# Kernel tuning notes

Hardware: AMD Instinct MI355X
Metric: run time of the kernel (lower is better)

Reference implementation:

```python
import jax, jax.numpy as jnp
import numpy as np
import math


def setup_inputs() -> dict:
    key = jax.random.key(0)
    k1, k2 = jax.random.split(key)
    q = jax.random.normal(k1, (2, 8, 2048, 64), dtype=jnp.float32)
    v = jax.random.normal(k2, (2, 8, 2048, 64), dtype=jnp.float32)
    return {"q": q, "v": v}


def reference(q, v):
    # q, v: [B, H, L, D]. Softmax-free Gaussian-kernel attention.
    # squared L2 distance via expanded form: ||qi||^2 + ||qj||^2 - 2 qi.qj
    # (same math as the original's broadcasted difference, without the
    #  O(B,H,L,L,D) intermediate)
    d = q.shape[-1]
    sq = jnp.sum(q * q, axis=-1)                      # [B, H, L]
    dots = jnp.einsum('bhid,bhjd->bhij', q, q)        # [B, H, L, L]
    sq_l2 = sq[..., :, None] + sq[..., None, :] - 2.0 * dots
    score = jnp.exp(-1.0 / (2.0 * math.sqrt(d)) * sq_l2)  # [B, H, L, L]
    return jnp.einsum('bhij,bhjd->bhid', score, v)    # [B, H, L, D]
```

## Files before the change

kernel.cpp:

```cpp
#include <hip/hip_runtime.h>
#include <hip/hip_bf16.h>
#include <stdint.h>

typedef __bf16 bf16_t;
typedef bf16_t bf16x8 __attribute__((ext_vector_type(8)));
typedef float f32x16 __attribute__((ext_vector_type(16)));
typedef float fvec4 __attribute__((ext_vector_type(4)));
typedef unsigned int u32x4v __attribute__((ext_vector_type(4)));

#define LEN 2048
#define DIM 64
#define QBLK 128
#define KVB 64

#define C_L8  0.18033688011112043f
#define C_L16 0.09016844005556021f

__device__ __forceinline__ float fexp2(float x) {
#if __has_builtin(__builtin_amdgcn_exp2f)
  return __builtin_amdgcn_exp2f(x);
#else
  return exp2f(x);
#endif
}

__device__ __forceinline__ unsigned pk2(float lo, float hi) {
  union { bf16_t h; unsigned short u; } a, b;
  a.h = (bf16_t)lo; b.h = (bf16_t)hi;
  return (unsigned)a.u | ((unsigned)b.u << 16);
}

__device__ __forceinline__ int sw(int row, int byte) {
  return row * 128 + (byte ^ ((row & 7) << 4));
}

__global__ __launch_bounds__(512, 2) void soft_attn(
    const float* __restrict__ q, const float* __restrict__ v,
    float* __restrict__ out) {
  __shared__ __align__(16) char smem[33280];

  const int tid    = threadIdx.x;
  const int lane   = tid & 63;
  const int wave   = tid >> 6;
  const int rg     = wave & 3;
  const int parity = wave >> 2;
  const int tp     = tid & 255;
  const int g      = lane >> 5;
  const int nn     = lane & 31;

  const int wg = ((blockIdx.x & 7) << 5) | (blockIdx.x >> 3);
  const int bh = wg >> 4;
  const int qb = wg & 15;

  const float* qh = q + (size_t)bh * LEN * DIM;
  const float* vh = v + (size_t)bh * LEN * DIM;

  char*  kbufp = smem + parity * 8192;
  char*  vbufp = smem + 16384 + parity * 8192;
  float* wkp   = (float*)(smem + 32768) + parity * 64;

  const int qrow = qb * QBLK + rg * 32 + nn;
  bf16x8 qf[4];
  float sq = 0.f;
  {
    const float* qp = qh + (size_t)qrow * DIM;
#pragma unroll
    for (int kc = 0; kc < 4; ++kc) {
      const int d0 = kc * 16 + g * 8;
      fvec4 x = *(const fvec4*)(qp + d0);
      fvec4 y = *(const fvec4*)(qp + d0 + 4);
      bf16x8 t;
#pragma unroll
      for (int e = 0; e < 4; ++e) {
        bf16_t h0 = (bf16_t)x[e]; t[e]     = h0; float f0 = (float)h0; sq += f0 * f0;
        bf16_t h1 = (bf16_t)y[e]; t[e + 4] = h1; float f1 = (float)h1; sq += f1 * f1;
      }
      qf[kc] = t;
    }
  }
  sq += __shfl_xor(sq, 32);
  const float hq = sq * C_L16;

  f32x16 acc0 = {};
  f32x16 acc1 = {};

  for (int it = 0; it < 16; ++it) {
    const int jt = it * 2 + parity;
    const float* kg = qh + (size_t)jt * KVB * DIM;
    const float* vg = vh + (size_t)jt * KVB * DIM;

    __syncthreads();

#pragma unroll
    for (int s = 0; s < 2; ++s) {
      const int c  = tp + 256 * s;
      const int j  = c >> 3;
      const int d0 = (c & 7) * 8;
      fvec4 x = *(const fvec4*)(kg + j * DIM + d0);
      fvec4 y = *(const fvec4*)(kg + j * DIM + d0 + 4);
      bf16x8 t; float p = 0.f;
#pragma unroll
      for (int e = 0; e < 4; ++e) {
        bf16_t h0 = (bf16_t)x[e]; t[e]     = h0; float f0 = (float)h0; p += f0 * f0;
        bf16_t h1 = (bf16_t)y[e]; t[e + 4] = h1; float f1 = (float)h1; p += f1 * f1;
      }
      *(bf16x8*)(kbufp + sw(j, d0 * 2)) = t;
      p += __shfl_xor(p, 1);
      p += __shfl_xor(p, 2);
      p += __shfl_xor(p, 4);
      if ((lane & 7) == 0) wkp[j] = fexp2(-p * C_L16);
    }

    __syncthreads();

    float vl[2][8];
    const int vd = tp & 63;
    const int vw = tp >> 6;
#pragma unroll
    for (int s = 0; s < 2; ++s) {
      const int j0 = vw * 8 + 32 * s;
      const float* vp = vg + j0 * DIM + vd;
#pragma unroll
      for (int r = 0; r < 8; ++r) vl[s][r] = vp[r * DIM];
    }

    bf16x8 af[4];
#pragma unroll
    for (int jsub = 0; jsub < 2; ++jsub) {
      f32x16 t = {};
#pragma unroll
      for (int kc = 0; kc < 4; ++kc) {
        bf16x8 kf = *(const bf16x8*)(kbufp + sw(jsub * 32 + nn, kc * 32 + g * 16));
        t = __builtin_amdgcn_mfma_f32_32x32x16_bf16(kf, qf[kc], t, 0, 0, 0);
      }
      unsigned P[8];
#pragma unroll
      for (int e = 0; e < 8; ++e) {
        float s0 = fexp2(__builtin_fmaf(t[2 * e],     C_L8, -hq));
        float s1 = fexp2(__builtin_fmaf(t[2 * e + 1], C_L8, -hq));
        P[e] = pk2(s0, s1);
      }
      asm volatile("v_permlane32_swap_b32 %0, %1" : "+v"(P[0]), "+v"(P[2]));
      asm volatile("v_permlane32_swap_b32 %0, %1" : "+v"(P[1]), "+v"(P[3]));
      asm volatile("v_permlane32_swap_b32 %0, %1" : "+v"(P[4]), "+v"(P[6]));
      asm volatile("v_permlane32_swap_b32 %0, %1" : "+v"(P[5]), "+v"(P[7]));
      u32x4v f0v = { P[0], P[1], P[2], P[3] };
      u32x4v f1v = { P[4], P[5], P[6], P[7] };
      af[jsub * 2]     = __builtin_bit_cast(bf16x8, f0v);
      af[jsub * 2 + 1] = __builtin_bit_cast(bf16x8, f1v);
    }

#pragma unroll
    for (int s = 0; s < 2; ++s) {
      const int j0 = vw * 8 + 32 * s;
      bf16x8 t;
#pragma unroll
      for (int r = 0; r < 8; ++r) {
        float w = wkp[j0 + r];
        t[r] = (bf16_t)(vl[s][r] * w);
      }
      *(bf16x8*)(vbufp + sw(vd, j0 * 2)) = t;
    }

    __syncthreads();

#pragma unroll
    for (int kc = 0; kc < 4; ++kc) {
      bf16x8 v0 = *(const bf16x8*)(vbufp + sw(nn,      kc * 32 + g * 16));
      bf16x8 v1 = *(const bf16x8*)(vbufp + sw(32 + nn, kc * 32 + g * 16));
      acc0 = __builtin_amdgcn_mfma_f32_32x32x16_bf16(af[kc], v0, acc0, 0, 0, 0);
      acc1 = __builtin_amdgcn_mfma_f32_32x32x16_bf16(af[kc], v1, acc1, 0, 0, 0);
    }
  }

  __syncthreads();
  float* xb = (float*)smem + rg * 2048;
  if (parity == 1) {
#pragma unroll
    for (int r = 0; r < 16; ++r) {
      xb[r * 64 + lane]        = acc0[r];
      xb[(16 + r) * 64 + lane] = acc1[r];
    }
  }
  __syncthreads();
  if (parity == 0) {
    float* op = out + ((size_t)bh * LEN + qb * QBLK + rg * 32) * DIM;
#pragma unroll
    for (int r = 0; r < 16; ++r) {
      const int row = (r & 3) + 8 * (r >> 2) + 4 * g;
      op[(size_t)row * DIM + nn]      = acc0[r] + xb[r * 64 + lane];
      op[(size_t)row * DIM + 32 + nn] = acc1[r] + xb[(16 + r) * 64 + lane];
    }
  }
}

extern "C" void kernel_launch(void* const* d_in, const int* in_sizes, int n_in,
                              void* d_out, int out_size, void* d_ws, size_t ws_size,
                              hipStream_t stream) {
  const float* q = (const float*)d_in[0];
  const float* v = (const float*)d_in[1];
  float* out = (float*)d_out;
  (void)in_sizes; (void)n_in; (void)d_ws; (void)ws_size; (void)out_size;
  soft_attn<<<dim3(256), dim3(512), 0, stream>>>(q, v, out);
}
```

Before: 106.5 us.

## Add bf16 prepass kernel and double-buffered async-LDS main attention kernel

Adds a prepass that converts Q/K to bf16 once, computes the squared norms, and stores V pre-scaled by exp(-||k||^2) and transposed into the workspace. The main kernel then streams bf16 K and V^T tiles directly into LDS through global_load_lds, double-buffered so the next tile loads while the current one computes. It splits the KV loop across four waves per query group and uses 64-row query blocks with 512 workgroups. The aim is to drop the per-block redundant fp32 conversion and the extra barriers. In exchange it pays for a second launch and a round trip through workspace memory, and it falls back to the old kernel when the workspace is too small.

```diff
diff --git a/kernel.cpp b/kernel.cpp
--- a/kernel.cpp
+++ b/kernel.cpp
@@ -10,8 +10,7 @@
 
 #define LEN 2048
 #define DIM 64
-#define QBLK 128
-#define KVB 64
+#define NH  16
 
 #define C_L8  0.18033688011112043f
 #define C_L16 0.09016844005556021f
@@ -30,36 +29,229 @@
   return (unsigned)a.u | ((unsigned)b.u << 16);
 }
 
-__device__ __forceinline__ int sw(int row, int byte) {
+__device__ __forceinline__ void glds16(const void* g, void* l) {
+  __builtin_amdgcn_global_load_lds(
+      (const __attribute__((address_space(1))) void*)g,
+      (__attribute__((address_space(3))) void*)l, 16, 0, 0);
+}
+
+__device__ __forceinline__ int swk(int row, int b) {
+  return row * 128 + (b ^ ((row & 7) << 4));
+}
+__device__ __forceinline__ int swv(int row, int b) {
+  return row * 256 + (b ^ ((row & 7) << 4));
+}
+
+__global__ __launch_bounds__(256) void prepass(
+    const float* __restrict__ q, const float* __restrict__ v,
+    bf16_t* __restrict__ kb, bf16_t* __restrict__ vt, float* __restrict__ sqw) {
+  __shared__ float wlds[64];
+  const int b = blockIdx.x;
+  const int h = b >> 5, jb = b & 31;
+  const int t = threadIdx.x;
+  const float* qh = q + ((size_t)h * LEN + jb * 64) * DIM;
+  const float* vh = v + ((size_t)h * LEN + jb * 64) * DIM;
+
+  {
+    const int j = t >> 2, d0 = (t & 3) * 16;
+    const float* qp = qh + j * DIM + d0;
+    float s = 0.f;
+    bf16x8 o0, o1;
+#pragma unroll
+    for (int e = 0; e < 8; ++e) {
+      bf16_t hh = (bf16_t)qp[e]; o0[e] = hh; float f = (float)hh; s += f * f;
+    }
+#pragma unroll
+    for (int e = 0; e < 8; ++e) {
+      bf16_t hh = (bf16_t)qp[8 + e]; o1[e] = hh; float f = (float)hh; s += f * f;
+    }
+    bf16_t* kp = kb + ((size_t)h * LEN + jb * 64 + j) * DIM + d0;
+    *(bf16x8*)kp = o0;
+    *(bf16x8*)(kp + 8) = o1;
+    s += __shfl_xor(s, 1);
+    s += __shfl_xor(s, 2);
+    if ((t & 3) == 0) {
+      wlds[j] = fexp2(-s * C_L16);
+      sqw[h * LEN + jb * 64 + j] = s * C_L16;
+    }
+  }
+  __syncthreads();
+  {
+    const int d = t & 63, jg = t >> 6;
+    float vv[16];
+#pragma unroll
+    for (int e = 0; e < 16; ++e) vv[e] = vh[(jg * 16 + e) * DIM + d];
+    bf16x8 o0, o1;
+#pragma unroll
+    for (int e = 0; e < 8; ++e)  o0[e] = (bf16_t)(vv[e] * wlds[jg * 16 + e]);
+#pragma unroll
+    for (int e = 0; e < 8; ++e)  o1[e] = (bf16_t)(vv[8 + e] * wlds[jg * 16 + 8 + e]);
+    bf16_t* vp = vt + ((size_t)h * DIM + d) * LEN + jb * 64 + jg * 16;
+    *(bf16x8*)vp = o0;
+    *(bf16x8*)(vp + 8) = o1;
+  }
+}
+
+__global__ __launch_bounds__(512, 4) void soft_attn_main(
+    const bf16_t* __restrict__ kb, const bf16_t* __restrict__ vt,
+    const float* __restrict__ sqw, float* __restrict__ out) {
+  __shared__ __align__(16) char smem[65536];
+
+  const int tid  = threadIdx.x;
+  const int lane = tid & 63;
+  const int wave = tid >> 6;
+  const int rg   = wave & 1;
+  const int par  = wave >> 1;
+  const int g    = lane >> 5;
+  const int nn   = lane & 31;
+
+  const int b  = blockIdx.x;
+  const int wg = ((b & 7) << 6) | (b >> 3);
+  const int bh = wg >> 5;
+  const int qb = wg & 31;
+
+  const bf16_t* kh  = kb + (size_t)bh * LEN * DIM;
+  const bf16_t* vth = vt + (size_t)bh * DIM * LEN;
+
+  const int qrow = qb * 64 + rg * 32 + nn;
+  bf16x8 qf[4];
+  {
+    const bf16_t* qp = kh + (size_t)qrow * DIM;
+#pragma unroll
+    for (int kc = 0; kc < 4; ++kc)
+      qf[kc] = *(const bf16x8*)(qp + kc * 16 + g * 8);
+  }
+  const float hq = sqw[bh * LEN + qrow];
+
+  const bf16_t* ksrc[2];
+  const bf16_t* vsrc[2];
+#pragma unroll
+  for (int s = 0; s < 2; ++s) {
+    const int krow = wave * 16 + s * 8 + (lane >> 3);
+    const int kby  = ((lane & 7) * 16) ^ ((lane >> 3) << 4);
+    ksrc[s] = kh + (size_t)krow * DIM + (kby >> 1);
+    const int vrow = wave * 8 + s * 4 + (lane >> 4);
+    const int vby  = ((lane & 15) * 16) ^ ((vrow & 7) << 4);
+    vsrc[s] = vth + (size_t)vrow * LEN + (vby >> 1);
+  }
+  char* kdst = smem + wave * 2048;
+  char* vdst = smem + 32768 + wave * 2048;
+
+  f32x16 acc0 = {};
+  f32x16 acc1 = {};
+
+#pragma unroll
+  for (int s = 0; s < 2; ++s) {
+    glds16(ksrc[s], kdst + s * 1024);
+    glds16(vsrc[s], vdst + s * 1024);
+  }
+  __syncthreads();
+
+  int buf = 0;
+  for (int it = 0; it < 16; ++it) {
+    if (it + 1 < 16) {
+      const int nb = buf ^ 1;
+#pragma unroll
+      for (int s = 0; s < 2; ++s) {
+        glds16(ksrc[s] + (size_t)(it + 1) * 128 * DIM, kdst + nb * 16384 + s * 1024);
+        glds16(vsrc[s] + (size_t)(it + 1) * 128,       vdst + nb * 16384 + s * 1024);
+      }
+    }
+
+    const char* kb0 = smem + buf * 16384;
+    const char* vb0 = smem + 32768 + buf * 16384;
+
+    f32x16 t = {};
+#pragma unroll
+    for (int kc = 0; kc < 4; ++kc) {
+      bf16x8 kf = *(const bf16x8*)(kb0 + swk(par * 32 + nn, kc * 32 + g * 16));
+      t = __builtin_amdgcn_mfma_f32_32x32x16_bf16(kf, qf[kc], t, 0, 0, 0);
+    }
+
+    unsigned P[8];
+#pragma unroll
+    for (int e = 0; e < 8; ++e) {
+      float s0 = fexp2(__builtin_fmaf(t[2 * e],     C_L8, -hq));
+      float s1 = fexp2(__builtin_fmaf(t[2 * e + 1], C_L8, -hq));
+      P[e] = pk2(s0, s1);
+    }
+    asm volatile("v_permlane32_swap_b32 %0, %1" : "+v"(P[0]), "+v"(P[2]));
+    asm volatile("v_permlane32_swap_b32 %0, %1" : "+v"(P[1]), "+v"(P[3]));
+    asm volatile("v_permlane32_swap_b32 %0, %1" : "+v"(P[4]), "+v"(P[6]));
+    asm volatile("v_permlane32_swap_b32 %0, %1" : "+v"(P[5]), "+v"(P[7]));
+    u32x4v f0v = { P[0], P[1], P[2], P[3] };
+    u32x4v f1v = { P[4], P[5], P[6], P[7] };
+    bf16x8 af0 = __builtin_bit_cast(bf16x8, f0v);
+    bf16x8 af1 = __builtin_bit_cast(bf16x8, f1v);
+
+    {
+      bf16x8 v0 = *(const bf16x8*)(vb0 + swv(nn,      par * 64 + g * 16));
+      bf16x8 v1 = *(const bf16x8*)(vb0 + swv(32 + nn, par * 64 + g * 16));
+      acc0 = __builtin_amdgcn_mfma_f32_32x32x16_bf16(af0, v0, acc0, 0, 0, 0);
+      acc1 = __builtin_amdgcn_mfma_f32_32x32x16_bf16(af0, v1, acc1, 0, 0, 0);
+      v0 = *(const bf16x8*)(vb0 + swv(nn,      par * 64 + 32 + g * 16));
+      v1 = *(const bf16x8*)(vb0 + swv(32 + nn, par * 64 + 32 + g * 16));
+      acc0 = __builtin_amdgcn_mfma_f32_32x32x16_bf16(af1, v0, acc0, 0, 0, 0);
+      acc1 = __builtin_amdgcn_mfma_f32_32x32x16_bf16(af1, v1, acc1, 0, 0, 0);
+    }
+
+    __syncthreads();
+    buf ^= 1;
+  }
+
+  float* xb = (float*)smem;
+  if (par != 0) {
+    float* dst = xb + ((par - 1) * 2 + rg) * 2048;
+#pragma unroll
+    for (int r = 0; r < 16; ++r) {
+      dst[r * 64 + lane]        = acc0[r];
+      dst[(16 + r) * 64 + lane] = acc1[r];
+    }
+  }
+  __syncthreads();
+  if (par == 0) {
+    float* op = out + ((size_t)bh * LEN + qb * 64 + rg * 32) * DIM;
+#pragma unroll
+    for (int r = 0; r < 16; ++r) {
+      const int row = (r & 3) + 8 * (r >> 2) + 4 * g;
+      float a0 = acc0[r], a1 = acc1[r];
+#pragma unroll
+      for (int p = 1; p < 4; ++p) {
+        const float* sb = xb + ((p - 1) * 2 + rg) * 2048;
+        a0 += sb[r * 64 + lane];
+        a1 += sb[(16 + r) * 64 + lane];
+      }
+      op[(size_t)row * DIM + nn]      = a0;
+      op[(size_t)row * DIM + 32 + nn] = a1;
+    }
+  }
+}
+
+__device__ __forceinline__ int swfb(int row, int byte) {
   return row * 128 + (byte ^ ((row & 7) << 4));
 }
 
-__global__ __launch_bounds__(512, 2) void soft_attn(
+__global__ __launch_bounds__(512, 2) void soft_attn_fb(
     const float* __restrict__ q, const float* __restrict__ v,
     float* __restrict__ out) {
   __shared__ __align__(16) char smem[33280];
-
-  const int tid    = threadIdx.x;
-  const int lane   = tid & 63;
-  const int wave   = tid >> 6;
-  const int rg     = wave & 3;
+  const int tid = threadIdx.x;
+  const int lane = tid & 63;
+  const int wave = tid >> 6;
+  const int rg = wave & 3;
   const int parity = wave >> 2;
-  const int tp     = tid & 255;
-  const int g      = lane >> 5;
-  const int nn     = lane & 31;
-
+  const int tp = tid & 255;
+  const int g = lane >> 5;
+  const int nn = lane & 31;
   const int wg = ((blockIdx.x & 7) << 5) | (blockIdx.x >> 3);
   const int bh = wg >> 4;
   const int qb = wg & 15;
-
   const float* qh = q + (size_t)bh * LEN * DIM;
   const float* vh = v + (size_t)bh * LEN * DIM;
-
-  char*  kbufp = smem + parity * 8192;
-  char*  vbufp = smem + 16384 + parity * 8192;
-  float* wkp   = (float*)(smem + 32768) + parity * 64;
-
-  const int qrow = qb * QBLK + rg * 32 + nn;
+  char* kbufp = smem + parity * 8192;
+  char* vbufp = smem + 16384 + parity * 8192;
+  float* wkp = (float*)(smem + 32768) + parity * 64;
+  const int qrow = qb * 128 + rg * 32 + nn;
   bf16x8 qf[4];
   float sq = 0.f;
   {
@@ -72,7 +264,7 @@
       bf16x8 t;
 #pragma unroll
       for (int e = 0; e < 4; ++e) {
-        bf16_t h0 = (bf16_t)x[e]; t[e]     = h0; float f0 = (float)h0; sq += f0 * f0;
+        bf16_t h0 = (bf16_t)x[e]; t[e] = h0; float f0 = (float)h0; sq += f0 * f0;
         bf16_t h1 = (bf16_t)y[e]; t[e + 4] = h1; float f1 = (float)h1; sq += f1 * f1;
       }
       qf[kc] = t;
@@ -80,39 +272,33 @@
   }
   sq += __shfl_xor(sq, 32);
   const float hq = sq * C_L16;
-
   f32x16 acc0 = {};
   f32x16 acc1 = {};
-
   for (int it = 0; it < 16; ++it) {
     const int jt = it * 2 + parity;
-    const float* kg = qh + (size_t)jt * KVB * DIM;
-    const float* vg = vh + (size_t)jt * KVB * DIM;
-
+    const float* kg = qh + (size_t)jt * 64 * DIM;
+    const float* vg = vh + (size_t)jt * 64 * DIM;
     __syncthreads();
-
 #pragma unroll
     for (int s = 0; s < 2; ++s) {
-      const int c  = tp + 256 * s;
-      const int j  = c >> 3;
+      const int c = tp + 256 * s;
+      const int j = c >> 3;
       const int d0 = (c & 7) * 8;
       fvec4 x = *(const fvec4*)(kg + j * DIM + d0);
       fvec4 y = *(const fvec4*)(kg + j * DIM + d0 + 4);
       bf16x8 t; float p = 0.f;
 #pragma unroll
       for (int e = 0; e < 4; ++e) {
-        bf16_t h0 = (bf16_t)x[e]; t[e]     = h0; float f0 = (float)h0; p += f0 * f0;
+        bf16_t h0 = (bf16_t)x[e]; t[e] = h0; float f0 = (float)h0; p += f0 * f0;
         bf16_t h1 = (bf16_t)y[e]; t[e + 4] = h1; float f1 = (float)h1; p += f1 * f1;
       }
-      *(bf16x8*)(kbufp + sw(j, d0 * 2)) = t;
+      *(bf16x8*)(kbufp + swfb(j, d0 * 2)) = t;
       p += __shfl_xor(p, 1);
       p += __shfl_xor(p, 2);
       p += __shfl_xor(p, 4);
       if ((lane & 7) == 0) wkp[j] = fexp2(-p * C_L16);
     }
-
     __syncthreads();
-
     float vl[2][8];
     const int vd = tp & 63;
     const int vw = tp >> 6;
@@ -123,20 +309,19 @@
 #pragma unroll
       for (int r = 0; r < 8; ++r) vl[s][r] = vp[r * DIM];
     }
-
     bf16x8 af[4];
 #pragma unroll
     for (int jsub = 0; jsub < 2; ++jsub) {
       f32x16 t = {};
 #pragma unroll
       for (int kc = 0; kc < 4; ++kc) {
-        bf16x8 kf = *(const bf16x8*)(kbufp + sw(jsub * 32 + nn, kc * 32 + g * 16));
+        bf16x8 kf = *(const bf16x8*)(kbufp + swfb(jsub * 32 + nn, kc * 32 + g * 16));
         t = __builtin_amdgcn_mfma_f32_32x32x16_bf16(kf, qf[kc], t, 0, 0, 0);
       }
       unsigned P[8];
 #pragma unroll
       for (int e = 0; e < 8; ++e) {
-        float s0 = fexp2(__builtin_fmaf(t[2 * e],     C_L8, -hq));
+        float s0 = fexp2(__builtin_fmaf(t[2 * e], C_L8, -hq));
         float s1 = fexp2(__builtin_fmaf(t[2 * e + 1], C_L8, -hq));
         P[e] = pk2(s0, s1);
       }
@@ -146,10 +331,9 @@
       asm volatile("v_permlane32_swap_b32 %0, %1" : "+v"(P[5]), "+v"(P[7]));
       u32x4v f0v = { P[0], P[1], P[2], P[3] };
       u32x4v f1v = { P[4], P[5], P[6], P[7] };
-      af[jsub * 2]     = __builtin_bit_cast(bf16x8, f0v);
+      af[jsub * 2] = __builtin_bit_cast(bf16x8, f0v);
       af[jsub * 2 + 1] = __builtin_bit_cast(bf16x8, f1v);
     }
-
 #pragma unroll
     for (int s = 0; s < 2; ++s) {
       const int j0 = vw * 8 + 32 * s;
@@ -159,36 +343,33 @@
         float w = wkp[j0 + r];
         t[r] = (bf16_t)(vl[s][r] * w);
       }
-      *(bf16x8*)(vbufp + sw(vd, j0 * 2)) = t;
-    }
-
+      *(bf16x8*)(vbufp + swfb(vd, j0 * 2)) = t;
+    }
     __syncthreads();
-
 #pragma unroll
     for (int kc = 0; kc < 4; ++kc) {
-      bf16x8 v0 = *(const bf16x8*)(vbufp + sw(nn,      kc * 32 + g * 16));
-      bf16x8 v1 = *(const bf16x8*)(vbufp + sw(32 + nn, kc * 32 + g * 16));
+      bf16x8 v0 = *(const bf16x8*)(vbufp + swfb(nn, kc * 32 + g * 16));
+      bf16x8 v1 = *(const bf16x8*)(vbufp + swfb(32 + nn, kc * 32 + g * 16));
       acc0 = __builtin_amdgcn_mfma_f32_32x32x16_bf16(af[kc], v0, acc0, 0, 0, 0);
       acc1 = __builtin_amdgcn_mfma_f32_32x32x16_bf16(af[kc], v1, acc1, 0, 0, 0);
     }
   }
-
   __syncthreads();
   float* xb = (float*)smem + rg * 2048;
   if (parity == 1) {
 #pragma unroll
     for (int r = 0; r < 16; ++r) {
-      xb[r * 64 + lane]        = acc0[r];
+      xb[r * 64 + lane] = acc0[r];
       xb[(16 + r) * 64 + lane] = acc1[r];
     }
   }
   __syncthreads();
   if (parity == 0) {
-    float* op = out + ((size_t)bh * LEN + qb * QBLK + rg * 32) * DIM;
+    float* op = out + ((size_t)bh * LEN + qb * 128 + rg * 32) * DIM;
 #pragma unroll
     for (int r = 0; r < 16; ++r) {
       const int row = (r & 3) + 8 * (r >> 2) + 4 * g;
-      op[(size_t)row * DIM + nn]      = acc0[r] + xb[r * 64 + lane];
+      op[(size_t)row * DIM + nn] = acc0[r] + xb[r * 64 + lane];
       op[(size_t)row * DIM + 32 + nn] = acc1[r] + xb[(16 + r) * 64 + lane];
     }
   }
@@ -200,6 +381,17 @@
   const float* q = (const float*)d_in[0];
   const float* v = (const float*)d_in[1];
   float* out = (float*)d_out;
-  (void)in_sizes; (void)n_in; (void)d_ws; (void)ws_size; (void)out_size;
-  soft_attn<<<dim3(256), dim3(512), 0, stream>>>(q, v, out);
-}
+  (void)in_sizes; (void)n_in; (void)out_size;
+
+  const size_t KB_BYTES = (size_t)NH * LEN * DIM * 2;
+  const size_t NEED = KB_BYTES * 2 + (size_t)NH * LEN * 4;
+  if (ws_size >= NEED) {
+    bf16_t* kb  = (bf16_t*)d_ws;
+    bf16_t* vt  = (bf16_t*)((char*)d_ws + KB_BYTES);
+    float*  sqw = (float*)((char*)d_ws + KB_BYTES * 2);
+    prepass<<<dim3(512), dim3(256), 0, stream>>>(q, v, kb, vt, sqw);
+    soft_attn_main<<<dim3(512), dim3(512), 0, stream>>>(kb, vt, sqw, out);
+  } else {
+    soft_attn_fb<<<dim3(256), dim3(512), 0, stream>>>(q, v, out);
+  }
+}
```

New measurement: 95.07 us. -10.7%, faster.
